# Kernel optimization log

Hardware: AMD Instinct MI355X
Metric: run time of the kernel (lower is better)

## Reference

```python
import jax, jax.numpy as jnp
import numpy as np

SQRT2 = 1.4142135623730951

def _gelu(x):
    return x * 0.5 * (1.0 + jax.lax.erf(x / SQRT2))

def _layer_norm(x, w, b, eps=1e-12):
    u = x.mean(-1, keepdims=True)
    s = ((x - u) ** 2).mean(-1, keepdims=True)
    return w * (x - u) / jnp.sqrt(s + eps) + b

def _rel_shift(x):
    # Transformer-XL relative shift: x is [b, n, q, p] -> shifted [b, n, q, p]
    b, n, q, p = x.shape
    x = jnp.concatenate([jnp.zeros((b, n, q, 1), x.dtype), x], axis=-1)
    x = x.reshape(b, n, p + 1, q)[:, :, 1:, :].reshape(b, n, q, p)
    return x

def setup_inputs() -> dict:
    key = jax.random.key(0)
    B, L, H, N = 4, 2048, 512, 8
    D = H // N
    ks = jax.random.split(key, 20)
    s = 0.02
    inp = {
        'x': jax.random.normal(ks[0], (B, L, H), jnp.float32),
        'pos_enc': jax.random.normal(ks[1], (L, H), jnp.float32),
        'Wq': jax.random.normal(ks[2], (N, H, D), jnp.float32) * s,
        'bq': jax.random.normal(ks[3], (N, D), jnp.float32) * s,
        'Wk': jax.random.normal(ks[4], (N, H, D), jnp.float32) * s,
        'bk': jax.random.normal(ks[5], (N, D), jnp.float32) * s,
        'Wv': jax.random.normal(ks[6], (N, H, D), jnp.float32) * s,
        'bv': jax.random.normal(ks[7], (N, D), jnp.float32) * s,
        'Wr': jax.random.normal(ks[8], (N, H, D), jnp.float32) * s,
        'br': jax.random.normal(ks[9], (N, D), jnp.float32) * s,
        'content_bias': jax.random.normal(ks[10], (N, D), jnp.float32) * s,
        'pos_bias': jax.random.normal(ks[11], (N, D), jnp.float32) * s,
        'Wc': jax.random.normal(ks[12], (H, H), jnp.float32) * s,
        'bc': jax.random.normal(ks[13], (H,), jnp.float32) * s,
        'W1': jax.random.normal(ks[14], (H, H), jnp.float32) * s,
        'b1': jax.random.normal(ks[15], (H,), jnp.float32) * s,
        'W2': jax.random.normal(ks[16], (H, H), jnp.float32) * s,
        'b2': jax.random.normal(ks[17], (H,), jnp.float32) * s,
        'ln_w': jnp.ones((H,), jnp.float32),
        'ln_b': jnp.zeros((H,), jnp.float32),
        # causal mask (True = masked out), as in subbatch_masks
        'mask': jnp.triu(jnp.ones((L, L), bool), k=1),
    }
    return inp

def reference(x, pos_enc, Wq, bq, Wk, bk, Wv, bv, Wr, br, content_bias, pos_bias,
              Wc, bc, W1, b1, W2, b2, ln_w, ln_b, mask):
    B, L, H = x.shape
    N, _, D = Wq.shape
    # per-head projections (LinearSplit)
    q = jnp.einsum('blh,nhd->bnld', x, Wq) + bq[None, :, None, :]
    k = jnp.einsum('blh,nhd->bnld', x, Wk) + bk[None, :, None, :]
    v = jnp.einsum('blh,nhd->bnld', x, Wv) + bv[None, :, None, :]
    r = jnp.einsum('ph,nhd->npd', pos_enc, Wr) + br[:, None, :]  # [n, L, d]
    qc = q + content_bias[None, :, None, :]
    qp = q + pos_bias[None, :, None, :]
    # content + relative-position biased scores (Transformer-XL)
    scores = jnp.einsum('bnid,bnjd->bnij', qc, k)
    scores = scores + _rel_shift(jnp.einsum('bnid,npd->bnip', qp, r))
    scores = scores / jnp.sqrt(jnp.asarray(D, scores.dtype))
    m = mask[None, None, :, :]
    scores = jnp.where(m, jnp.finfo(scores.dtype).min, scores)
    w = jax.nn.softmax(scores, axis=-1)
    w = jnp.where(m, 0.0, w)
    out = jnp.einsum('bnij,bnjd->bnid', w, v)
    out = out.transpose(0, 2, 1, 3).reshape(B, L, H)
    a = out @ Wc.T + bc
    a = _layer_norm(a + x, ln_w, ln_b)
    h = _gelu(a @ W1.T + b1) @ W2.T + b2
    return _layer_norm(a + h, ln_w, ln_b)
```

## Files before the change

### kernel.cpp

```cpp
#include <hip/hip_runtime.h>
#include <math.h>

#define HDIM 512
#define LSEQ 2048
#define NH 8
#define DH 64
#define NEGBIG (-3.0e38f)

#define MODE_QDUAL  0
#define MODE_KV     1
#define MODE_VT     2
#define MODE_RE     3
#define MODE_F32RES 4
#define MODE_GELU   5

typedef short bf16x8 __attribute__((ext_vector_type(8)));
typedef float f32x4 __attribute__((ext_vector_type(4)));

__device__ __forceinline__ unsigned short f2b(float f) {
  union { float f; unsigned u; } x; x.f = f;
  unsigned r = x.u + 0x7FFF + ((x.u >> 16) & 1);
  return (unsigned short)(r >> 16);
}
__device__ __forceinline__ float b2f(unsigned short u) {
  union { unsigned u; float f; } x; x.u = ((unsigned)u) << 16;
  return x.f;
}

__device__ __forceinline__ void gl_lds16(const void* g, void* l) {
  __builtin_amdgcn_global_load_lds(
      (const __attribute__((address_space(1))) void*)g,
      (__attribute__((address_space(3))) void*)l, 16, 0, 0);
}

__global__ __launch_bounds__(256) void conv_f32_bf16(
    const float* __restrict__ in, unsigned short* __restrict__ out, int n4)
{
  int idx = blockIdx.x * 256 + threadIdx.x;
  if (idx < n4) {
    float4 v = ((const float4*)in)[idx];
    ushort4 o; o.x = f2b(v.x); o.y = f2b(v.y); o.z = f2b(v.z); o.w = f2b(v.w);
    ((ushort4*)out)[idx] = o;
  }
}

__global__ __launch_bounds__(256) void conv_weights(
    const float* __restrict__ Wq, const float* __restrict__ Wk,
    const float* __restrict__ Wv, const float* __restrict__ Wr,
    const float* __restrict__ Wc, const float* __restrict__ W1,
    const float* __restrict__ W2, unsigned short* __restrict__ wT)
{
  const int widx = blockIdx.y;
  const float* src = (widx == 0) ? Wq : (widx == 1) ? Wk : (widx == 2) ? Wv :
                     (widx == 3) ? Wr : (widx == 4) ? Wc : (widx == 5) ? W1 : W2;
  unsigned short* dst = wT + (size_t)widx * 262144;
  const int t = threadIdx.x;
  const int tile = blockIdx.x;

  if (widx < 4) {
    __shared__ float td[64][65];
    const int h0 = (tile >> 3) * 64;
    const int n  = tile & 7;
    #pragma unroll
    for (int it = 0; it < 4; ++it) {
      int row = it * 16 + (t >> 4), dc = (t & 15) * 4;
      float4 v = *(const float4*)(src + (size_t)n * 32768 + (size_t)(h0 + row) * 64 + dc);
      td[row][dc] = v.x; td[row][dc + 1] = v.y; td[row][dc + 2] = v.z; td[row][dc + 3] = v.w;
    }
    __syncthreads();
    #pragma unroll
    for (int it = 0; it < 4; ++it) {
      int d = it * 16 + (t >> 4), h4 = (t & 15) * 4;
      ushort4 o;
      o.x = f2b(td[h4 + 0][d]); o.y = f2b(td[h4 + 1][d]);
      o.z = f2b(td[h4 + 2][d]); o.w = f2b(td[h4 + 3][d]);
      *(ushort4*)(dst + (size_t)(n * 64 + d) * 512 + h0 + h4) = o;
    }
  } else {
    #pragma unroll
    for (int i = 0; i < 4; ++i) {
      int f4 = tile * 1024 + i * 256 + t;
      float4 v = ((const float4*)src)[f4];
      ushort4 o; o.x = f2b(v.x); o.y = f2b(v.y); o.z = f2b(v.z); o.w = f2b(v.w);
      ((ushort4*)dst)[f4] = o;
    }
  }
}

__device__ __forceinline__ void gemm_core(
    const unsigned short* __restrict__ A, const unsigned short* __restrict__ BT,
    const float* __restrict__ bias, const float* __restrict__ cb2,
    const float* __restrict__ pb2, const float* __restrict__ resf,
    const unsigned short* __restrict__ res16,
    void* __restrict__ C1v, unsigned short* __restrict__ C2, int mode,
    int bx, int by, char* SMEM)
{
  unsigned short* As = (unsigned short*)SMEM;
  unsigned short* Bs = (unsigned short*)(SMEM + 16384);

  const int t = threadIdx.x;
  const int w = t >> 6, lane = t & 63;
  const int l15 = lane & 15, quad = lane >> 4;
  const int r0 = by * 128;
  const int c0 = bx * 64;
  const int wm = (w >> 1) * 64, wc = (w & 1) * 32;

  f32x4 acc[4][2];
  #pragma unroll
  for (int sr = 0; sr < 4; ++sr)
    #pragma unroll
    for (int sc = 0; sc < 2; ++sc) acc[sr][sc] = (f32x4){0.f, 0.f, 0.f, 0.f};

  const int sub = lane >> 3;
  const int g   = (lane & 7) ^ sub;

  for (int k0 = 0; k0 < 512; k0 += 64) {
    __syncthreads();
    #pragma unroll
    for (int i = 0; i < 4; ++i) {
      int rowb = w * 32 + i * 8;
      gl_lds16(A + (size_t)(r0 + rowb + sub) * 512 + k0 + g * 8, As + rowb * 64);
    }
    #pragma unroll
    for (int i = 0; i < 2; ++i) {
      int rowb = w * 16 + i * 8;
      gl_lds16(BT + (size_t)(c0 + rowb + sub) * 512 + k0 + g * 8, Bs + rowb * 64);
    }
    __syncthreads();

    #pragma unroll
    for (int kk = 0; kk < 2; ++kk) {
      bf16x8 af[4], bf[2];
      #pragma unroll
      for (int s = 0; s < 4; ++s) {
        int ar = wm + s * 16 + l15;
        af[s] = *(const bf16x8*)(As + ar * 64 + (((quad + 4 * kk) ^ (ar & 7)) << 3));
      }
      #pragma unroll
      for (int s = 0; s < 2; ++s) {
        int br = wc + s * 16 + l15;
        bf[s] = *(const bf16x8*)(Bs + br * 64 + (((quad + 4 * kk) ^ (br & 7)) << 3));
      }
      #pragma unroll
      for (int sr = 0; sr < 4; ++sr)
        #pragma unroll
        for (int sc = 0; sc < 2; ++sc)
          acc[sr][sc] = __builtin_amdgcn_mfma_f32_16x16x32_bf16(
              af[sr], bf[sc], acc[sr][sc], 0, 0, 0);
    }
  }

  __syncthreads();

  unsigned short* C1u = (unsigned short*)C1v;
  float* C1f = (float*)C1v;

  if (mode == MODE_F32RES) {
    float* LDf = (float*)SMEM;
    #pragma unroll
    for (int h = 0; h < 2; ++h) {
      if ((w >> 1) == h) {
        #pragma unroll
        for (int sc = 0; sc < 2; ++sc) {
          int cl = wc + sc * 16 + l15;
          float bia = bias[c0 + cl];
          #pragma unroll
          for (int sr = 0; sr < 4; ++sr)
            #pragma unroll
            for (int r = 0; r < 4; ++r) {
              int ml = sr * 16 + quad * 4 + r;
              LDf[ml * 68 + cl] = acc[sr][sc][r] + bia;
            }
        }
      }
      __syncthreads();
      int row = t >> 2, m = r0 + h * 64 + row;
      #pragma unroll
      for (int j = 0; j < 4; ++j) {
        int col = (t & 3) * 16 + j * 4;
        float4 vv = *(const float4*)(LDf + row * 68 + col);
        size_t gofs = (size_t)m * 512 + c0 + col;
        if (resf) {
          float4 rr = *(const float4*)(resf + gofs);
          vv.x += rr.x; vv.y += rr.y; vv.z += rr.z; vv.w += rr.w;
        } else if (res16) {
          ushort4 rv = *(const ushort4*)(res16 + gofs);
          vv.x += b2f(rv.x); vv.y += b2f(rv.y); vv.z += b2f(rv.z); vv.w += b2f(rv.w);
        }
        *(float4*)(C1f + gofs) = vv;
      }
      __syncthreads();
    }
  } else if (mode == MODE_VT) {
    unsigned short* LDb = (unsigned short*)SMEM;
    #pragma unroll
    for (int sc = 0; sc < 2; ++sc) {
      int cl = wc + sc * 16 + l15;
      float bia = bias[c0 + cl];
      #pragma unroll
      for (int sr = 0; sr < 4; ++sr)
        #pragma unroll
        for (int r = 0; r < 4; ++r) {
          int ml = wm + sr * 16 + quad * 4 + r;
          LDb[cl * 136 + ml] = f2b(acc[sr][sc][r] + bia);
        }
    }
    __syncthreads();
    int row = t >> 2;
    int c = c0 + row, n = c >> 6, d = c & 63;
    #pragma unroll
    for (int j = 0; j < 4; ++j) {
      int mcol = (t & 3) * 32 + j * 8;
      int4 val = *(const int4*)(LDb + row * 136 + mcol);
      int m = r0 + mcol, bb = m >> 11, l = m & 2047;
      *(int4*)(C1u + ((size_t)(bb * NH + n) * DH + d) * LSEQ + l) = val;
    }
  } else {
    unsigned short* LDb = (unsigned short*)SMEM;
    const int passes = (mode == MODE_QDUAL) ? 2 : 1;
    for (int p = 0; p < passes; ++p) {
      #pragma unroll
      for (int sc = 0; sc < 2; ++sc) {
        int cl = wc + sc * 16 + l15;
        int c = c0 + cl;
        float bia = bias[c];
        float ex = (mode == MODE_QDUAL) ? ((p == 0) ? cb2[c] : pb2[c]) : 0.f;
        #pragma unroll
        for (int sr = 0; sr < 4; ++sr)
          #pragma unroll
          for (int r = 0; r < 4; ++r) {
            int ml = wm + sr * 16 + quad * 4 + r;
            float v = acc[sr][sc][r] + bia;
            if (mode == MODE_QDUAL) v = (v + ex) * 0.125f;
            if (mode == MODE_GELU)
              v = 0.5f * v * (1.0f + erff(v * 0.70710678118654752f));
            LDb[ml * 72 + cl] = f2b(v);
          }
      }
      __syncthreads();
      int row = t >> 1;
      #pragma unroll
      for (int j = 0; j < 4; ++j) {
        int col = (t & 1) * 32 + j * 8;
        int4 val = *(const int4*)(LDb + row * 72 + col);
        unsigned short* dst;
        int c = c0 + col, n = c >> 6, d = c & 63;
        if (mode == MODE_RE) {
          int m = r0 + row;
          dst = C1u + ((size_t)n * LSEQ + (LSEQ - 1 - m)) * DH + d;
        } else if (mode == MODE_GELU) {
          dst = C1u + (size_t)(r0 + row) * 512 + c0 + col;
        } else {
          int m = r0 + row, bb = m >> 11, l = m & 2047;
          dst = ((p == 0) ? C1u : C2) + ((size_t)(bb * NH + n) * LSEQ + l) * DH + d;
        }
        *(int4*)dst = val;
      }
      if (p + 1 < passes) __syncthreads();
    }
  }
}

__global__ __launch_bounds__(256) void gemm_mfma(
    const unsigned short* __restrict__ A, const unsigned short* __restrict__ BT,
    const float* __restrict__ bias, const float* __restrict__ resf,
    const unsigned short* __restrict__ res16,
    void* __restrict__ C1v, int mode)
{
  __shared__ __align__(16) char SMEM[24576];
  gemm_core(A, BT, bias, nullptr, nullptr, resf, res16, C1v, nullptr, mode,
            blockIdx.x, blockIdx.y, SMEM);
}

__global__ __launch_bounds__(256) void qkv_fused(
    const unsigned short* __restrict__ xb, const unsigned short* __restrict__ posb,
    const unsigned short* __restrict__ WqT, const unsigned short* __restrict__ WkT,
    const unsigned short* __restrict__ WvT, const unsigned short* __restrict__ WrT,
    const float* __restrict__ bq, const float* __restrict__ bk,
    const float* __restrict__ bv, const float* __restrict__ br,
    const float* __restrict__ cbv, const float* __restrict__ pbv,
    unsigned short* __restrict__ qcb, unsigned short* __restrict__ qpb,
    unsigned short* __restrict__ kbb, unsigned short* __restrict__ vtb,
    unsigned short* __restrict__ rebb)
{
  __shared__ __align__(16) char SMEM[24576];
  const int z = blockIdx.z;
  if (z == 0) {
    gemm_core(xb, WqT, bq, cbv, pbv, nullptr, nullptr, qcb, qpb, MODE_QDUAL,
              blockIdx.x, blockIdx.y, SMEM);
  } else if (z == 1) {
    gemm_core(xb, WkT, bk, nullptr, nullptr, nullptr, nullptr, kbb, nullptr, MODE_KV,
              blockIdx.x, blockIdx.y, SMEM);
  } else if (z == 2) {
    gemm_core(xb, WvT, bv, nullptr, nullptr, nullptr, nullptr, vtb, nullptr, MODE_VT,
              blockIdx.x, blockIdx.y, SMEM);
  } else {
    if (blockIdx.y >= 16) return;
    gemm_core(posb, WrT, br, nullptr, nullptr, nullptr, nullptr, rebb, nullptr, MODE_RE,
              blockIdx.x, blockIdx.y, SMEM);
  }
}

#define PROW(i) ((i) * 72 + (((i) >> 2) << 3))

__global__ __launch_bounds__(256, 3) void attn_mfma(
    const unsigned short* __restrict__ qcb, const unsigned short* __restrict__ qpb,
    const unsigned short* __restrict__ kbb, const unsigned short* __restrict__ vtb,
    const unsigned short* __restrict__ rebb, unsigned short* __restrict__ outb)
{
  __shared__ __align__(16) unsigned short Ks[64 * 72];
  __shared__ __align__(16) unsigned short Vts[64 * 72];
  __shared__ __align__(16) unsigned short Res[128 * 72];
  __shared__ __align__(16) unsigned short TPb[4 * 16 * 84];

  const int t = threadIdx.x;
  const int bn = blockIdx.x;
  const int b = bn >> 3, n = bn & 7;
  const int ib = 31 - blockIdx.y;
  const int i0 = ib * 64;
  const int w = t >> 6;
  const int lane = t & 63;
  const int l15 = lane & 15, quad = lane >> 4;

  bf16x8 qcf[2], qpf[2];
  {
    size_t base = ((size_t)bn * LSEQ + i0 + 16 * w + l15) * DH + quad * 8;
    qcf[0] = *(const bf16x8*)(qcb + base);
    qcf[1] = *(const bf16x8*)(qcb + base + 32);
    qpf[0] = *(const bf16x8*)(qpb + base);
    qpf[1] = *(const bf16x8*)(qpb + base + 32);
  }

  f32x4 Of[4];
  #pragma unroll
  for (int s = 0; s < 4; ++s) Of[s] = (f32x4){0.f, 0.f, 0.f, 0.f};
  float lsum[4] = {0.f, 0.f, 0.f, 0.f};

  unsigned short* Tw = TPb + w * 1344;
  const int Ibase = i0 + 16 * w;
  const int nt = ib + 1;

  const int r2 = t >> 2, gl2 = t & 3;
  const int r1 = t >> 1, h1 = t & 1;

  for (int tt = 0; tt < nt; ++tt) {
    const int j0 = tt * 64;
    const int db = i0 - j0;

    const int4* skp = (const int4*)(kbb + ((size_t)bn * LSEQ + j0 + r2) * DH + gl2 * 16);
    int4 ka0 = skp[0], ka1 = skp[1];
    const int4* svp = (const int4*)(vtb + ((size_t)bn * DH + r2) * LSEQ + j0 + gl2 * 16);
    int4 va0 = svp[0], va1 = svp[1];
    int dist = db - 63 + r1;
    int4 ra[2][2];
    #pragma unroll
    for (int gi = 0; gi < 2; ++gi) {
      if (dist >= 0 && dist < LSEQ) {
        const int4* srp = (const int4*)(rebb + ((size_t)n * LSEQ + dist) * DH + (h1 * 2 + gi) * 16);
        ra[gi][0] = srp[0]; ra[gi][1] = srp[1];
      } else {
        int4 z = {0, 0, 0, 0};
        ra[gi][0] = z; ra[gi][1] = z;
      }
    }
    __syncthreads();
    {
      unsigned short* dk = Ks + r2 * 72 + ((gl2 ^ (r2 & 3)) * 16);
      *(int4*)(dk) = ka0; *(int4*)(dk + 8) = ka1;
      unsigned short* dv = Vts + r2 * 72 + ((gl2 ^ (r2 & 3)) * 16);
      *(int4*)(dv) = va0; *(int4*)(dv + 8) = va1;
      #pragma unroll
      for (int gi = 0; gi < 2; ++gi) {
        int gl = h1 * 2 + gi;
        unsigned short* dr = Res + r1 * 72 + ((gl ^ (r1 & 3)) * 16);
        *(int4*)(dr) = ra[gi][0]; *(int4*)(dr + 8) = ra[gi][1];
      }
    }
    __syncthreads();

    f32x4 Sf[4];
    #pragma unroll
    for (int s = 0; s < 4; ++s) {
      f32x4 acc = {0.f, 0.f, 0.f, 0.f};
      int row = 16 * s + l15;
      #pragma unroll
      for (int kk = 0; kk < 2; ++kk) {
        int g = (quad >> 1) + 2 * kk;
        bf16x8 bfr = *(const bf16x8*)(Ks + row * 72 + ((g ^ (row & 3)) * 16) + (quad & 1) * 8);
        acc = __builtin_amdgcn_mfma_f32_16x16x32_bf16(qcf[kk], bfr, acc, 0, 0, 0);
      }
      Sf[s] = acc;
    }
    #pragma unroll
    for (int s = 0; s < 5; ++s) {
      f32x4 acc = {0.f, 0.f, 0.f, 0.f};
      int row = 16 * w + 16 * s + l15;
      #pragma unroll
      for (int kk = 0; kk < 2; ++kk) {
        int g = (quad >> 1) + 2 * kk;
        bf16x8 bfr = *(const bf16x8*)(Res + row * 72 + ((g ^ (row & 3)) * 16) + (quad & 1) * 8);
        acc = __builtin_amdgcn_mfma_f32_16x16x32_bf16(qpf[kk], bfr, acc, 0, 0, 0);
      }
      #pragma unroll
      for (int r = 0; r < 4; ++r) {
        int i = quad * 4 + r;
        Tw[i * 84 + 16 * s + l15] = f2b(acc[r]);
      }
    }
    asm volatile("s_waitcnt lgkmcnt(0)" ::: "memory");

    float p_s[4][4];
    #pragma unroll
    for (int s = 0; s < 4; ++s)
      #pragma unroll
      for (int r = 0; r < 4; ++r) {
        int i = quad * 4 + r;
        float tval = b2f(Tw[i * 84 + 63 + i - 16 * s - l15]);
        float v = Sf[s][r] + tval;
        int j = j0 + 16 * s + l15;
        float p = (j <= Ibase + i) ? __expf(v) : 0.0f;
        p_s[s][r] = p;
        lsum[r] += p;
      }
    #pragma unroll
    for (int s = 0; s < 4; ++s)
      #pragma unroll
      for (int r = 0; r < 4; ++r) {
        int i = quad * 4 + r;
        Tw[PROW(i) + ((s ^ (i & 3)) * 16) + l15] = f2b(p_s[s][r]);
      }
    asm volatile("s_waitcnt lgkmcnt(0)" ::: "memory");

    #pragma unroll
    for (int kk = 0; kk < 2; ++kk) {
      int g = (quad >> 1) + 2 * kk;
      bf16x8 pa = *(const bf16x8*)(Tw + PROW(l15) + ((g ^ (l15 & 3)) * 16) + (quad & 1) * 8);
      #pragma unroll
      for (int s = 0; s < 4; ++s) {
        int d = 16 * s + l15;
        bf16x8 vb8 = *(const bf16x8*)(Vts + d * 72 + ((g ^ (d & 3)) * 16) + (quad & 1) * 8);
        Of[s] = __builtin_amdgcn_mfma_f32_16x16x32_bf16(pa, vb8, Of[s], 0, 0, 0);
      }
    }
  }

  #pragma unroll
  for (int r = 0; r < 4; ++r) {
    float rs = lsum[r];
    rs += __shfl_xor(rs, 1, 64);
    rs += __shfl_xor(rs, 2, 64);
    rs += __shfl_xor(rs, 4, 64);
    rs += __shfl_xor(rs, 8, 64);
    float linv = 1.0f / rs;
    int I = Ibase + quad * 4 + r;
    size_t base = ((size_t)b * LSEQ + I) * HDIM + n * DH;
    #pragma unroll
    for (int s = 0; s < 4; ++s)
      outb[base + 16 * s + l15] = f2b(Of[s][r] * linv);
  }
}

__global__ __launch_bounds__(256) void ln_kernel(
    const float* __restrict__ xin, const float* __restrict__ w,
    const float* __restrict__ bb, float* __restrict__ outf,
    unsigned short* __restrict__ out16)
{
  __shared__ float red[8];
  const int row = blockIdx.x, t = threadIdx.x;
  const size_t base = (size_t)row * 512;
  float v0 = xin[base + t], v1 = xin[base + t + 256];
  float s = v0 + v1;
  #pragma unroll
  for (int off = 32; off >= 1; off >>= 1) s += __shfl_xor(s, off, 64);
  if ((t & 63) == 0) red[t >> 6] = s;
  __syncthreads();
  float mean = (red[0] + red[1] + red[2] + red[3]) * (1.0f / 512.0f);
  float d0 = v0 - mean, d1 = v1 - mean;
  float s2 = d0 * d0 + d1 * d1;
  #pragma unroll
  for (int off = 32; off >= 1; off >>= 1) s2 += __shfl_xor(s2, off, 64);
  if ((t & 63) == 0) red[4 + (t >> 6)] = s2;
  __syncthreads();
  float var = (red[4] + red[5] + red[6] + red[7]) * (1.0f / 512.0f);
  float inv = 1.0f / sqrtf(var + 1e-12f);
  float o0 = w[t] * d0 * inv + bb[t];
  float o1 = w[t + 256] * d1 * inv + bb[t + 256];
  if (outf)  { outf[base + t] = o0; outf[base + t + 256] = o1; }
  if (out16) { out16[base + t] = f2b(o0); out16[base + t + 256] = f2b(o1); }
}

extern "C" void kernel_launch(void* const* d_in, const int* in_sizes, int n_in,
                              void* d_out, int out_size, void* d_ws, size_t ws_size,
                              hipStream_t stream)
{
  (void)in_sizes; (void)n_in; (void)out_size; (void)ws_size;
  const float* x   = (const float*)d_in[0];
  const float* pos = (const float*)d_in[1];
  const float* Wq  = (const float*)d_in[2];
  const float* bq  = (const float*)d_in[3];
  const float* Wk  = (const float*)d_in[4];
  const float* bk  = (const float*)d_in[5];
  const float* Wv  = (const float*)d_in[6];
  const float* bv  = (const float*)d_in[7];
  const float* Wr  = (const float*)d_in[8];
  const float* br  = (const float*)d_in[9];
  const float* cbv = (const float*)d_in[10];
  const float* pbv = (const float*)d_in[11];
  const float* Wc  = (const float*)d_in[12];
  const float* bc  = (const float*)d_in[13];
  const float* W1  = (const float*)d_in[14];
  const float* b1  = (const float*)d_in[15];
  const float* W2  = (const float*)d_in[16];
  const float* b2  = (const float*)d_in[17];
  const float* lnw = (const float*)d_in[18];
  const float* lnb = (const float*)d_in[19];
  char* ws = (char*)d_ws;
  float* outp = (float*)d_out;

  unsigned short* xb   = (unsigned short*)(ws);
  unsigned short* posb = (unsigned short*)(ws + 8388608);
  unsigned short* wT   = (unsigned short*)(ws + 10485760);
  unsigned short* qcb  = (unsigned short*)(ws + 14155776);
  unsigned short* qpb  = (unsigned short*)(ws + 22544384);
  unsigned short* kbb  = (unsigned short*)(ws + 30932992);
  unsigned short* vtb  = (unsigned short*)(ws + 39321600);
  unsigned short* rebb = (unsigned short*)(ws + 47710208);
  unsigned short* WqT = wT;
  unsigned short* WkT = wT + 262144;
  unsigned short* WvT = wT + 2 * 262144;
  unsigned short* WrT = wT + 3 * 262144;
  unsigned short* WcT = wT + 4 * 262144;
  unsigned short* W1T = wT + 5 * 262144;
  unsigned short* W2T = wT + 6 * 262144;
  unsigned short* attnb = (unsigned short*)d_out;
  float*          cpre  = (float*)(ws + 14155776);
  unsigned short* ab16  = (unsigned short*)(ws);
  unsigned short* h1b   = (unsigned short*)(ws + 30932992);
  float*          h2pre = (float*)(ws + 14155776);

  dim3 blk(256);
  dim3 g8(8, 64);

  conv_f32_bf16<<<4096, blk, 0, stream>>>(x, xb, 1048576);
  conv_f32_bf16<<<1024, blk, 0, stream>>>(pos, posb, 262144);
  conv_weights<<<dim3(64, 7), blk, 0, stream>>>(Wq, Wk, Wv, Wr, Wc, W1, W2, wT);

  qkv_fused<<<dim3(8, 64, 4), blk, 0, stream>>>(
      xb, posb, WqT, WkT, WvT, WrT, bq, bk, bv, br, cbv, pbv,
      qcb, qpb, kbb, vtb, rebb);

  attn_mfma<<<dim3(32, 32), blk, 0, stream>>>(qcb, qpb, kbb, vtb, rebb, attnb);

  gemm_mfma<<<g8, blk, 0, stream>>>(attnb, WcT, bc, x, nullptr, cpre, MODE_F32RES);
  ln_kernel<<<8192, blk, 0, stream>>>(cpre, lnw, lnb, nullptr, ab16);
  gemm_mfma<<<g8, blk, 0, stream>>>(ab16, W1T, b1, nullptr, nullptr, h1b, MODE_GELU);
  gemm_mfma<<<g8, blk, 0, stream>>>(h1b, W2T, b2, nullptr, ab16, h2pre, MODE_F32RES);
  ln_kernel<<<8192, blk, 0, stream>>>(h2pre, lnw, lnb, outp, nullptr);
}
```

Measured before the change: 317.2 us.

## Read K, V and R fragments directly from global memory, dropping LDS staging

```diff
diff --git a/kernel.cpp b/kernel.cpp
--- a/kernel.cpp
+++ b/kernel.cpp
@@ -6,6 +6,7 @@
 #define NH 8
 #define DH 64
 #define NEGBIG (-3.0e38f)
+#define REPITCH 2111
 
 #define MODE_QDUAL  0
 #define MODE_KV     1
@@ -247,7 +248,7 @@
         int c = c0 + col, n = c >> 6, d = c & 63;
         if (mode == MODE_RE) {
           int m = r0 + row;
-          dst = C1u + ((size_t)n * LSEQ + (LSEQ - 1 - m)) * DH + d;
+          dst = C1u + ((size_t)n * REPITCH + 63 + (LSEQ - 1 - m)) * DH + d;
         } else if (mode == MODE_GELU) {
           dst = C1u + (size_t)(r0 + row) * 512 + c0 + col;
         } else {
@@ -295,7 +296,19 @@
     gemm_core(xb, WvT, bv, nullptr, nullptr, nullptr, nullptr, vtb, nullptr, MODE_VT,
               blockIdx.x, blockIdx.y, SMEM);
   } else {
-    if (blockIdx.y >= 16) return;
+    if (blockIdx.y == 16) {
+      int4 z4 = {0, 0, 0, 0};
+      for (int it = 0; it < 16; ++it) {
+        int tid = threadIdx.x + 256 * it;
+        if (tid < 504 * 8) {
+          int rowi = tid >> 3, chunk = tid & 7;
+          int n = rowi / 63, gr = rowi - n * 63;
+          *(int4*)(rebb + ((size_t)n * REPITCH + gr) * DH + chunk * 8) = z4;
+        }
+      }
+      return;
+    }
+    if (blockIdx.y > 16) return;
     gemm_core(posb, WrT, br, nullptr, nullptr, nullptr, nullptr, rebb, nullptr, MODE_RE,
               blockIdx.x, blockIdx.y, SMEM);
   }
@@ -303,14 +316,11 @@
 
 #define PROW(i) ((i) * 72 + (((i) >> 2) << 3))
 
-__global__ __launch_bounds__(256, 3) void attn_mfma(
+__global__ __launch_bounds__(256, 4) void attn_mfma(
     const unsigned short* __restrict__ qcb, const unsigned short* __restrict__ qpb,
     const unsigned short* __restrict__ kbb, const unsigned short* __restrict__ vtb,
     const unsigned short* __restrict__ rebb, unsigned short* __restrict__ outb)
 {
-  __shared__ __align__(16) unsigned short Ks[64 * 72];
-  __shared__ __align__(16) unsigned short Vts[64 * 72];
-  __shared__ __align__(16) unsigned short Res[128 * 72];
   __shared__ __align__(16) unsigned short TPb[4 * 16 * 84];
 
   const int t = threadIdx.x;
@@ -340,67 +350,34 @@
   const int Ibase = i0 + 16 * w;
   const int nt = ib + 1;
 
-  const int r2 = t >> 2, gl2 = t & 3;
-  const int r1 = t >> 1, h1 = t & 1;
+  const unsigned short* Kbase = kbb + ((size_t)bn * LSEQ + 16 * 0) * DH;
+  const unsigned short* Vbase = vtb + (size_t)bn * DH * LSEQ;
+  const unsigned short* Rbase = rebb + ((size_t)n * REPITCH + 63) * DH;
 
   for (int tt = 0; tt < nt; ++tt) {
     const int j0 = tt * 64;
     const int db = i0 - j0;
 
-    const int4* skp = (const int4*)(kbb + ((size_t)bn * LSEQ + j0 + r2) * DH + gl2 * 16);
-    int4 ka0 = skp[0], ka1 = skp[1];
-    const int4* svp = (const int4*)(vtb + ((size_t)bn * DH + r2) * LSEQ + j0 + gl2 * 16);
-    int4 va0 = svp[0], va1 = svp[1];
-    int dist = db - 63 + r1;
-    int4 ra[2][2];
-    #pragma unroll
-    for (int gi = 0; gi < 2; ++gi) {
-      if (dist >= 0 && dist < LSEQ) {
-        const int4* srp = (const int4*)(rebb + ((size_t)n * LSEQ + dist) * DH + (h1 * 2 + gi) * 16);
-        ra[gi][0] = srp[0]; ra[gi][1] = srp[1];
-      } else {
-        int4 z = {0, 0, 0, 0};
-        ra[gi][0] = z; ra[gi][1] = z;
-      }
-    }
-    __syncthreads();
-    {
-      unsigned short* dk = Ks + r2 * 72 + ((gl2 ^ (r2 & 3)) * 16);
-      *(int4*)(dk) = ka0; *(int4*)(dk + 8) = ka1;
-      unsigned short* dv = Vts + r2 * 72 + ((gl2 ^ (r2 & 3)) * 16);
-      *(int4*)(dv) = va0; *(int4*)(dv + 8) = va1;
-      #pragma unroll
-      for (int gi = 0; gi < 2; ++gi) {
-        int gl = h1 * 2 + gi;
-        unsigned short* dr = Res + r1 * 72 + ((gl ^ (r1 & 3)) * 16);
-        *(int4*)(dr) = ra[gi][0]; *(int4*)(dr + 8) = ra[gi][1];
-      }
-    }
-    __syncthreads();
-
     f32x4 Sf[4];
     #pragma unroll
     for (int s = 0; s < 4; ++s) {
       f32x4 acc = {0.f, 0.f, 0.f, 0.f};
-      int row = 16 * s + l15;
-      #pragma unroll
-      for (int kk = 0; kk < 2; ++kk) {
-        int g = (quad >> 1) + 2 * kk;
-        bf16x8 bfr = *(const bf16x8*)(Ks + row * 72 + ((g ^ (row & 3)) * 16) + (quad & 1) * 8);
-        acc = __builtin_amdgcn_mfma_f32_16x16x32_bf16(qcf[kk], bfr, acc, 0, 0, 0);
-      }
+      const unsigned short* kr = Kbase + (size_t)(j0 + 16 * s + l15) * DH + quad * 8;
+      #pragma unroll
+      for (int kk = 0; kk < 2; ++kk)
+        acc = __builtin_amdgcn_mfma_f32_16x16x32_bf16(
+            qcf[kk], *(const bf16x8*)(kr + kk * 32), acc, 0, 0, 0);
       Sf[s] = acc;
     }
     #pragma unroll
     for (int s = 0; s < 5; ++s) {
       f32x4 acc = {0.f, 0.f, 0.f, 0.f};
-      int row = 16 * w + 16 * s + l15;
-      #pragma unroll
-      for (int kk = 0; kk < 2; ++kk) {
-        int g = (quad >> 1) + 2 * kk;
-        bf16x8 bfr = *(const bf16x8*)(Res + row * 72 + ((g ^ (row & 3)) * 16) + (quad & 1) * 8);
-        acc = __builtin_amdgcn_mfma_f32_16x16x32_bf16(qpf[kk], bfr, acc, 0, 0, 0);
-      }
+      int dist = db - 63 + 16 * w + 16 * s + l15;
+      const unsigned short* rr = Rbase + (long)dist * DH + quad * 8;
+      #pragma unroll
+      for (int kk = 0; kk < 2; ++kk)
+        acc = __builtin_amdgcn_mfma_f32_16x16x32_bf16(
+            qpf[kk], *(const bf16x8*)(rr + kk * 32), acc, 0, 0, 0);
       #pragma unroll
       for (int r = 0; r < 4; ++r) {
         int i = quad * 4 + r;
@@ -437,9 +414,9 @@
       bf16x8 pa = *(const bf16x8*)(Tw + PROW(l15) + ((g ^ (l15 & 3)) * 16) + (quad & 1) * 8);
       #pragma unroll
       for (int s = 0; s < 4; ++s) {
-        int d = 16 * s + l15;
-        bf16x8 vb8 = *(const bf16x8*)(Vts + d * 72 + ((g ^ (d & 3)) * 16) + (quad & 1) * 8);
-        Of[s] = __builtin_amdgcn_mfma_f32_16x16x32_bf16(pa, vb8, Of[s], 0, 0, 0);
+        const unsigned short* vr = Vbase + (size_t)(16 * s + l15) * LSEQ + j0 + kk * 32 + quad * 8;
+        Of[s] = __builtin_amdgcn_mfma_f32_16x16x32_bf16(
+            pa, *(const bf16x8*)vr, Of[s], 0, 0, 0);
       }
     }
   }
```

Result: slower. 490.3 us (+54.6%).

## Store residual pre-LN activations in bf16, wave-per-row LayerNorm, merge conversion kernels

Applied to the files above, without the earlier changes.

```diff
diff --git a/kernel.cpp b/kernel.cpp
--- a/kernel.cpp
+++ b/kernel.cpp
@@ -11,7 +11,7 @@
 #define MODE_KV     1
 #define MODE_VT     2
 #define MODE_RE     3
-#define MODE_F32RES 4
+#define MODE_B16RES 4
 #define MODE_GELU   5
 
 typedef short bf16x8 __attribute__((ext_vector_type(8)));
@@ -33,56 +33,63 @@
       (__attribute__((address_space(3))) void*)l, 16, 0, 0);
 }
 
-__global__ __launch_bounds__(256) void conv_f32_bf16(
-    const float* __restrict__ in, unsigned short* __restrict__ out, int n4)
-{
-  int idx = blockIdx.x * 256 + threadIdx.x;
-  if (idx < n4) {
-    float4 v = ((const float4*)in)[idx];
-    ushort4 o; o.x = f2b(v.x); o.y = f2b(v.y); o.z = f2b(v.z); o.w = f2b(v.w);
-    ((ushort4*)out)[idx] = o;
-  }
-}
-
-__global__ __launch_bounds__(256) void conv_weights(
+__global__ __launch_bounds__(256) void conv_all(
+    const float* __restrict__ x, const float* __restrict__ pos,
     const float* __restrict__ Wq, const float* __restrict__ Wk,
     const float* __restrict__ Wv, const float* __restrict__ Wr,
     const float* __restrict__ Wc, const float* __restrict__ W1,
-    const float* __restrict__ W2, unsigned short* __restrict__ wT)
-{
-  const int widx = blockIdx.y;
-  const float* src = (widx == 0) ? Wq : (widx == 1) ? Wk : (widx == 2) ? Wv :
-                     (widx == 3) ? Wr : (widx == 4) ? Wc : (widx == 5) ? W1 : W2;
-  unsigned short* dst = wT + (size_t)widx * 262144;
+    const float* __restrict__ W2,
+    unsigned short* __restrict__ xb, unsigned short* __restrict__ posb,
+    unsigned short* __restrict__ wT)
+{
   const int t = threadIdx.x;
-  const int tile = blockIdx.x;
-
-  if (widx < 4) {
-    __shared__ float td[64][65];
-    const int h0 = (tile >> 3) * 64;
-    const int n  = tile & 7;
-    #pragma unroll
-    for (int it = 0; it < 4; ++it) {
-      int row = it * 16 + (t >> 4), dc = (t & 15) * 4;
-      float4 v = *(const float4*)(src + (size_t)n * 32768 + (size_t)(h0 + row) * 64 + dc);
-      td[row][dc] = v.x; td[row][dc + 1] = v.y; td[row][dc + 2] = v.z; td[row][dc + 3] = v.w;
-    }
-    __syncthreads();
-    #pragma unroll
-    for (int it = 0; it < 4; ++it) {
-      int d = it * 16 + (t >> 4), h4 = (t & 15) * 4;
-      ushort4 o;
-      o.x = f2b(td[h4 + 0][d]); o.y = f2b(td[h4 + 1][d]);
-      o.z = f2b(td[h4 + 2][d]); o.w = f2b(td[h4 + 3][d]);
-      *(ushort4*)(dst + (size_t)(n * 64 + d) * 512 + h0 + h4) = o;
+  const int z = blockIdx.z;
+  if (z == 0) {
+    int idx = blockIdx.x * 256 + t;
+    float4 v = ((const float4*)x)[idx];
+    ushort4 o; o.x = f2b(v.x); o.y = f2b(v.y); o.z = f2b(v.z); o.w = f2b(v.w);
+    ((ushort4*)xb)[idx] = o;
+  } else if (z == 1) {
+    int idx = blockIdx.x * 256 + t;
+    if (idx < 262144) {
+      float4 v = ((const float4*)pos)[idx];
+      ushort4 o; o.x = f2b(v.x); o.y = f2b(v.y); o.z = f2b(v.z); o.w = f2b(v.w);
+      ((ushort4*)posb)[idx] = o;
     }
   } else {
-    #pragma unroll
-    for (int i = 0; i < 4; ++i) {
-      int f4 = tile * 1024 + i * 256 + t;
-      float4 v = ((const float4*)src)[f4];
-      ushort4 o; o.x = f2b(v.x); o.y = f2b(v.y); o.z = f2b(v.z); o.w = f2b(v.w);
-      ((ushort4*)dst)[f4] = o;
+    if (blockIdx.x >= 448) return;
+    const int widx = blockIdx.x >> 6;
+    const int tile = blockIdx.x & 63;
+    const float* src = (widx == 0) ? Wq : (widx == 1) ? Wk : (widx == 2) ? Wv :
+                       (widx == 3) ? Wr : (widx == 4) ? Wc : (widx == 5) ? W1 : W2;
+    unsigned short* dst = wT + (size_t)widx * 262144;
+    if (widx < 4) {
+      __shared__ float td[64][65];
+      const int h0 = (tile >> 3) * 64;
+      const int n  = tile & 7;
+      #pragma unroll
+      for (int it = 0; it < 4; ++it) {
+        int row = it * 16 + (t >> 4), dc = (t & 15) * 4;
+        float4 v = *(const float4*)(src + (size_t)n * 32768 + (size_t)(h0 + row) * 64 + dc);
+        td[row][dc] = v.x; td[row][dc + 1] = v.y; td[row][dc + 2] = v.z; td[row][dc + 3] = v.w;
+      }
+      __syncthreads();
+      #pragma unroll
+      for (int it = 0; it < 4; ++it) {
+        int d = it * 16 + (t >> 4), h4 = (t & 15) * 4;
+        ushort4 o;
+        o.x = f2b(td[h4 + 0][d]); o.y = f2b(td[h4 + 1][d]);
+        o.z = f2b(td[h4 + 2][d]); o.w = f2b(td[h4 + 3][d]);
+        *(ushort4*)(dst + (size_t)(n * 64 + d) * 512 + h0 + h4) = o;
+      }
+    } else {
+      #pragma unroll
+      for (int i = 0; i < 4; ++i) {
+        int f4 = tile * 1024 + i * 256 + t;
+        float4 v = ((const float4*)src)[f4];
+        ushort4 o; o.x = f2b(v.x); o.y = f2b(v.y); o.z = f2b(v.z); o.w = f2b(v.w);
+        ((ushort4*)dst)[f4] = o;
+      }
     }
   }
 }
@@ -153,45 +160,8 @@
   __syncthreads();
 
   unsigned short* C1u = (unsigned short*)C1v;
-  float* C1f = (float*)C1v;
-
-  if (mode == MODE_F32RES) {
-    float* LDf = (float*)SMEM;
-    #pragma unroll
-    for (int h = 0; h < 2; ++h) {
-      if ((w >> 1) == h) {
-        #pragma unroll
-        for (int sc = 0; sc < 2; ++sc) {
-          int cl = wc + sc * 16 + l15;
-          float bia = bias[c0 + cl];
-          #pragma unroll
-          for (int sr = 0; sr < 4; ++sr)
-            #pragma unroll
-            for (int r = 0; r < 4; ++r) {
-              int ml = sr * 16 + quad * 4 + r;
-              LDf[ml * 68 + cl] = acc[sr][sc][r] + bia;
-            }
-        }
-      }
-      __syncthreads();
-      int row = t >> 2, m = r0 + h * 64 + row;
-      #pragma unroll
-      for (int j = 0; j < 4; ++j) {
-        int col = (t & 3) * 16 + j * 4;
-        float4 vv = *(const float4*)(LDf + row * 68 + col);
-        size_t gofs = (size_t)m * 512 + c0 + col;
-        if (resf) {
-          float4 rr = *(const float4*)(resf + gofs);
-          vv.x += rr.x; vv.y += rr.y; vv.z += rr.z; vv.w += rr.w;
-        } else if (res16) {
-          ushort4 rv = *(const ushort4*)(res16 + gofs);
-          vv.x += b2f(rv.x); vv.y += b2f(rv.y); vv.z += b2f(rv.z); vv.w += b2f(rv.w);
-        }
-        *(float4*)(C1f + gofs) = vv;
-      }
-      __syncthreads();
-    }
-  } else if (mode == MODE_VT) {
+
+  if (mode == MODE_VT) {
     unsigned short* LDb = (unsigned short*)SMEM;
     #pragma unroll
     for (int sc = 0; sc < 2; ++sc) {
@@ -250,6 +220,28 @@
           dst = C1u + ((size_t)n * LSEQ + (LSEQ - 1 - m)) * DH + d;
         } else if (mode == MODE_GELU) {
           dst = C1u + (size_t)(r0 + row) * 512 + c0 + col;
+        } else if (mode == MODE_B16RES) {
+          int m = r0 + row;
+          size_t gofs = (size_t)m * 512 + c0 + col;
+          unsigned short tmp[8];
+          *(int4*)tmp = val;
+          if (resf) {
+            float4 ra = *(const float4*)(resf + gofs);
+            float4 rb = *(const float4*)(resf + gofs + 4);
+            tmp[0] = f2b(b2f(tmp[0]) + ra.x); tmp[1] = f2b(b2f(tmp[1]) + ra.y);
+            tmp[2] = f2b(b2f(tmp[2]) + ra.z); tmp[3] = f2b(b2f(tmp[3]) + ra.w);
+            tmp[4] = f2b(b2f(tmp[4]) + rb.x); tmp[5] = f2b(b2f(tmp[5]) + rb.y);
+            tmp[6] = f2b(b2f(tmp[6]) + rb.z); tmp[7] = f2b(b2f(tmp[7]) + rb.w);
+          } else {
+            ushort4 sa = *(const ushort4*)(res16 + gofs);
+            ushort4 sb = *(const ushort4*)(res16 + gofs + 4);
+            tmp[0] = f2b(b2f(tmp[0]) + b2f(sa.x)); tmp[1] = f2b(b2f(tmp[1]) + b2f(sa.y));
+            tmp[2] = f2b(b2f(tmp[2]) + b2f(sa.z)); tmp[3] = f2b(b2f(tmp[3]) + b2f(sa.w));
+            tmp[4] = f2b(b2f(tmp[4]) + b2f(sb.x)); tmp[5] = f2b(b2f(tmp[5]) + b2f(sb.y));
+            tmp[6] = f2b(b2f(tmp[6]) + b2f(sb.z)); tmp[7] = f2b(b2f(tmp[7]) + b2f(sb.w));
+          }
+          val = *(int4*)tmp;
+          dst = C1u + gofs;
         } else {
           int m = r0 + row, bb = m >> 11, l = m & 2047;
           dst = ((p == 0) ? C1u : C2) + ((size_t)(bb * NH + n) * LSEQ + l) * DH + d;
@@ -460,33 +452,56 @@
   }
 }
 
-__global__ __launch_bounds__(256) void ln_kernel(
-    const float* __restrict__ xin, const float* __restrict__ w,
+__global__ __launch_bounds__(256) void ln_b16(
+    const unsigned short* __restrict__ xin, const float* __restrict__ w,
     const float* __restrict__ bb, float* __restrict__ outf,
     unsigned short* __restrict__ out16)
 {
-  __shared__ float red[8];
-  const int row = blockIdx.x, t = threadIdx.x;
-  const size_t base = (size_t)row * 512;
-  float v0 = xin[base + t], v1 = xin[base + t + 256];
-  float s = v0 + v1;
+  const int t = threadIdx.x;
+  const int lane = t & 63;
+  const int row = blockIdx.x * 4 + (t >> 6);
+  const size_t base = (size_t)row * 512 + lane * 8;
+
+  unsigned short v16[8];
+  *(int4*)v16 = *(const int4*)(xin + base);
+  float v[8];
+  float s = 0.f;
+  #pragma unroll
+  for (int i = 0; i < 8; ++i) { v[i] = b2f(v16[i]); s += v[i]; }
   #pragma unroll
   for (int off = 32; off >= 1; off >>= 1) s += __shfl_xor(s, off, 64);
-  if ((t & 63) == 0) red[t >> 6] = s;
-  __syncthreads();
-  float mean = (red[0] + red[1] + red[2] + red[3]) * (1.0f / 512.0f);
-  float d0 = v0 - mean, d1 = v1 - mean;
-  float s2 = d0 * d0 + d1 * d1;
+  float mean = s * (1.0f / 512.0f);
+  float s2 = 0.f;
+  #pragma unroll
+  for (int i = 0; i < 8; ++i) { float d = v[i] - mean; s2 += d * d; }
   #pragma unroll
   for (int off = 32; off >= 1; off >>= 1) s2 += __shfl_xor(s2, off, 64);
-  if ((t & 63) == 0) red[4 + (t >> 6)] = s2;
-  __syncthreads();
-  float var = (red[4] + red[5] + red[6] + red[7]) * (1.0f / 512.0f);
-  float inv = 1.0f / sqrtf(var + 1e-12f);
-  float o0 = w[t] * d0 * inv + bb[t];
-  float o1 = w[t + 256] * d1 * inv + bb[t + 256];
-  if (outf)  { outf[base + t] = o0; outf[base + t + 256] = o1; }
-  if (out16) { out16[base + t] = f2b(o0); out16[base + t + 256] = f2b(o1); }
+  float inv = 1.0f / sqrtf(s2 * (1.0f / 512.0f) + 1e-12f);
+
+  float4 wa = *(const float4*)(w + lane * 8);
+  float4 wb = *(const float4*)(w + lane * 8 + 4);
+  float4 ba = *(const float4*)(bb + lane * 8);
+  float4 bbv = *(const float4*)(bb + lane * 8 + 4);
+  float o[8];
+  o[0] = wa.x * (v[0] - mean) * inv + ba.x;
+  o[1] = wa.y * (v[1] - mean) * inv + ba.y;
+  o[2] = wa.z * (v[2] - mean) * inv + ba.z;
+  o[3] = wa.w * (v[3] - mean) * inv + ba.w;
+  o[4] = wb.x * (v[4] - mean) * inv + bbv.x;
+  o[5] = wb.y * (v[5] - mean) * inv + bbv.y;
+  o[6] = wb.z * (v[6] - mean) * inv + bbv.z;
+  o[7] = wb.w * (v[7] - mean) * inv + bbv.w;
+  if (outf) {
+    float4 f0 = {o[0], o[1], o[2], o[3]}, f1 = {o[4], o[5], o[6], o[7]};
+    *(float4*)(outf + base) = f0;
+    *(float4*)(outf + base + 4) = f1;
+  }
+  if (out16) {
+    unsigned short u[8];
+    #pragma unroll
+    for (int i = 0; i < 8; ++i) u[i] = f2b(o[i]);
+    *(int4*)(out16 + base) = *(int4*)u;
+  }
 }
 
 extern "C" void kernel_launch(void* const* d_in, const int* in_sizes, int n_in,
@@ -532,18 +547,17 @@
   unsigned short* WcT = wT + 4 * 262144;
   unsigned short* W1T = wT + 5 * 262144;
   unsigned short* W2T = wT + 6 * 262144;
-  unsigned short* attnb = (unsigned short*)d_out;
-  float*          cpre  = (float*)(ws + 14155776);
-  unsigned short* ab16  = (unsigned short*)(ws);
-  unsigned short* h1b   = (unsigned short*)(ws + 30932992);
-  float*          h2pre = (float*)(ws + 14155776);
+  unsigned short* attnb  = (unsigned short*)d_out;
+  unsigned short* cpre16 = (unsigned short*)(ws + 14155776);
+  unsigned short* ab16   = (unsigned short*)(ws);
+  unsigned short* h1b    = (unsigned short*)(ws + 30932992);
+  unsigned short* h2b16  = (unsigned short*)(ws + 22544384);
 
   dim3 blk(256);
   dim3 g8(8, 64);
 
-  conv_f32_bf16<<<4096, blk, 0, stream>>>(x, xb, 1048576);
-  conv_f32_bf16<<<1024, blk, 0, stream>>>(pos, posb, 262144);
-  conv_weights<<<dim3(64, 7), blk, 0, stream>>>(Wq, Wk, Wv, Wr, Wc, W1, W2, wT);
+  conv_all<<<dim3(4096, 1, 3), blk, 0, stream>>>(
+      x, pos, Wq, Wk, Wv, Wr, Wc, W1, W2, xb, posb, wT);
 
   qkv_fused<<<dim3(8, 64, 4), blk, 0, stream>>>(
       xb, posb, WqT, WkT, WvT, WrT, bq, bk, bv, br, cbv, pbv,
@@ -551,9 +565,9 @@
 
   attn_mfma<<<dim3(32, 32), blk, 0, stream>>>(qcb, qpb, kbb, vtb, rebb, attnb);
 
-  gemm_mfma<<<g8, blk, 0, stream>>>(attnb, WcT, bc, x, nullptr, cpre, MODE_F32RES);
-  ln_kernel<<<8192, blk, 0, stream>>>(cpre, lnw, lnb, nullptr, ab16);
+  gemm_mfma<<<g8, blk, 0, stream>>>(attnb, WcT, bc, x, nullptr, cpre16, MODE_B16RES);
+  ln_b16<<<2048, blk, 0, stream>>>(cpre16, lnw, lnb, nullptr, ab16);
   gemm_mfma<<<g8, blk, 0, stream>>>(ab16, W1T, b1, nullptr, nullptr, h1b, MODE_GELU);
-  gemm_mfma<<<g8, blk, 0, stream>>>(h1b, W2T, b2, nullptr, ab16, h2pre, MODE_F32RES);
-  ln_kernel<<<8192, blk, 0, stream>>>(h2pre, lnw, lnb, outp, nullptr);
-}
+  gemm_mfma<<<g8, blk, 0, stream>>>(h1b, W2T, b2, nullptr, ab16, h2b16, MODE_B16RES);
+  ln_b16<<<2048, blk, 0, stream>>>(h2b16, lnw, lnb, outp, nullptr);
+}
```

Measured after the change: 309.2 us. 1.03x faster.
